# Kernel tuning notes

Measured on AMD Instinct MI355X. Metric: run time of the kernel, lower is better.

Reference implementation:

```python
import jax, jax.numpy as jnp
import numpy as np

K = 20
EPS = 1e-5


def _knn_idx(x, k):
    # x: (B, C, N) -> indices of k nearest neighbors (B, N, k)
    xx = jnp.sum(x * x, axis=1)                       # (B, N)
    inner = jnp.einsum('bcn,bcm->bnm', x, x)          # (B, N, N)
    pd = -xx[:, :, None] + 2.0 * inner - xx[:, None, :]  # negative sq dist
    return jax.lax.top_k(pd, k)[1]


def _graph_feature(x, k):
    # x: (B, C, N) -> (B, 2C, N, k) edge features [x_j - x_i, x_i]
    B = x.shape[0]
    idx = _knn_idx(x, k)                              # (B, N, k)
    xt = jnp.transpose(x, (0, 2, 1))                  # (B, N, C)
    feat = xt[jnp.arange(B)[:, None, None], idx]      # (B, N, k, C)
    center = jnp.broadcast_to(xt[:, :, None, :], feat.shape)
    e = jnp.concatenate([feat - center, center], axis=-1)
    return jnp.transpose(e, (0, 3, 1, 2))


def _bn2d(x, g, b):
    # training-mode BatchNorm2d: stats over (B, N, k)
    m = x.mean(axis=(0, 2, 3), keepdims=True)
    v = x.var(axis=(0, 2, 3), keepdims=True)
    return (x - m) / jnp.sqrt(v + EPS) * g[None, :, None, None] + b[None, :, None, None]


def _gn(x, g, b, groups):
    # GroupNorm on (B, C, N)
    B, C, N = x.shape
    xr = x.reshape(B, groups, C // groups, N)
    m = xr.mean(axis=(2, 3), keepdims=True)
    v = xr.var(axis=(2, 3), keepdims=True)
    xn = ((xr - m) / jnp.sqrt(v + EPS)).reshape(B, C, N)
    return xn * g[None, :, None] + b[None, :, None]


def _lrelu(x):
    return jnp.where(x >= 0, x, 0.2 * x)


def _edge_block(x, W, g, b, k):
    # kNN graph -> 1x1 conv -> BN -> LeakyReLU -> max over neighbors
    e = _graph_feature(x, k)                          # (B, 2C, N, k)
    y = jnp.einsum('oc,bcnk->bonk', W, e)
    return _lrelu(_bn2d(y, g, b)).max(axis=-1)        # (B, O, N)


def _encoder(x, W1, g1, b1, W2, g2, b2, W3, g3, b3, W4, g4, b4, W5, g5, b5,
             Wm1, bm1, gm1, hm1, Wm2, bm2, gm2, hm2, Wm3, bm3, gm3, hm3):
    B, _, N = x.shape
    x1 = _edge_block(x,  W1, g1, b1, K)               # (B,  64, N)
    x2 = _edge_block(x1, W2, g2, b2, K)               # (B,  64, N)
    x3 = _edge_block(x2, W3, g3, b3, K)               # (B, 128, N)
    x4 = _edge_block(x3, W4, g4, b4, K)               # (B, 256, N)
    loc = jnp.concatenate([x1, x2, x3, x4], axis=1)   # (B, 512, N)
    y = _lrelu(_gn(jnp.einsum('oc,bcn->bon', W5, loc), g5, b5, 32))  # (B,256,N)
    glb = jnp.concatenate([y.max(axis=-1), y.mean(axis=-1)], axis=1)  # (B,512)
    rep = jnp.broadcast_to(glb[:, :, None], (B, glb.shape[1], N))
    z = jnp.concatenate([loc, rep], axis=1)           # (B, 1024, N)
    z = jax.nn.relu(_gn(jnp.einsum('oc,bcn->bon', Wm1, z) + bm1[None, :, None], gm1, hm1, 32))
    z = jax.nn.relu(_gn(jnp.einsum('oc,bcn->bon', Wm2, z) + bm2[None, :, None], gm2, hm2, 32))
    emb = jax.nn.relu(_gn(jnp.einsum('oc,bcn->bon', Wm3, z) + bm3[None, :, None], gm3, hm3, 32))
    return emb, glb[:, :, None]


def setup_inputs():
    key = jax.random.key(0)
    ks = jax.random.split(key, 12)
    B, N = 8, 2048
    d = {}
    d['transpose_xyz'] = jax.random.normal(ks[0], (B, 3, N), dtype=jnp.float32)
    def w(k, o, c):
        return jax.random.normal(k, (o, c), dtype=jnp.float32) * (1.0 / np.sqrt(c).astype(np.float32))
    d['W1'] = w(ks[1], 64, 6);    d['g1'] = jnp.ones((64,), jnp.float32);  d['b1'] = jnp.zeros((64,), jnp.float32)
    d['W2'] = w(ks[2], 64, 128);  d['g2'] = jnp.ones((64,), jnp.float32);  d['b2'] = jnp.zeros((64,), jnp.float32)
    d['W3'] = w(ks[3], 128, 128); d['g3'] = jnp.ones((128,), jnp.float32); d['b3'] = jnp.zeros((128,), jnp.float32)
    d['W4'] = w(ks[4], 256, 256); d['g4'] = jnp.ones((256,), jnp.float32); d['b4'] = jnp.zeros((256,), jnp.float32)
    d['W5'] = w(ks[5], 256, 512); d['g5'] = jnp.ones((256,), jnp.float32); d['b5'] = jnp.zeros((256,), jnp.float32)
    d['Wm1'] = w(ks[6], 512, 1024); d['bm1'] = jnp.zeros((512,), jnp.float32); d['gm1'] = jnp.ones((512,), jnp.float32); d['hm1'] = jnp.zeros((512,), jnp.float32)
    d['Wm2'] = w(ks[7], 256, 512);  d['bm2'] = jnp.zeros((256,), jnp.float32); d['gm2'] = jnp.ones((256,), jnp.float32); d['hm2'] = jnp.zeros((256,), jnp.float32)
    d['Wm3'] = w(ks[8], 128, 256);  d['bm3'] = jnp.zeros((128,), jnp.float32); d['gm3'] = jnp.ones((128,), jnp.float32); d['hm3'] = jnp.zeros((128,), jnp.float32)
    return d


def reference(transpose_xyz, W1, g1, b1, W2, g2, b2, W3, g3, b3, W4, g4, b4,
              W5, g5, b5, Wm1, bm1, gm1, hm1, Wm2, bm2, gm2, hm2, Wm3, bm3, gm3, hm3):
    return _encoder(transpose_xyz, W1, g1, b1, W2, g2, b2, W3, g3, b3, W4, g4, b4,
                    W5, g5, b5, Wm1, bm1, gm1, hm1, Wm2, bm2, gm2, hm2, Wm3, bm3, gm3, hm3)
```

## Files before the change

kernel.cpp:

```cpp
#include <hip/hip_runtime.h>
#include <math.h>

#define B_SZ 8
#define NP   2048
#define KNN  20
#define CNT_F 327680.0f

#define OB_LOC   0ull
#define OB_RB    33554432ull
#define OB_RC    75497472ull
#define OB_RD    92274688ull
#define OB_X0    100663296ull
#define OB_XX    100925440ull
#define OB_STD   100990976ull
#define OB_STI   102301696ull
#define OB_PS    103612416ull
#define OB_MEAN  103613440ull
#define OB_VAR   103613568ull
#define OB_GLB   103613696ull
#define OB_T1    103630080ull
#define OB_GM    103646464ull
#define OB_GR    103647488ull

__global__ __launch_bounds__(256) void k_prep(const float* __restrict__ xin, float* __restrict__ x0) {
    int t = blockIdx.x * 256 + threadIdx.x;
    if (t >= B_SZ * NP) return;
    int b = t >> 11, n = t & 2047;
    const float* s = xin + (size_t)b * 3 * NP + n;
    ((float4*)x0)[t] = make_float4(s[0], s[NP], s[2 * NP], 0.f);
}

template <int C>
__global__ __launch_bounds__(256) void k_xx(const float* __restrict__ x, int rs, float* __restrict__ xx) {
    int t = blockIdx.x * 256 + threadIdx.x;
    if (t >= B_SZ * NP) return;
    const float* p = x + (size_t)t * rs;
    float s = 0.f;
    for (int c = 0; c < C; ++c) s = __fadd_rn(s, __fmul_rn(p[c], p[c]));
    xx[t] = s;
}

__global__ __launch_bounds__(256) void k_pds(const float* __restrict__ x, int rs, int K,
                                             const float* __restrict__ xx, int j0,
                                             float* __restrict__ S) {
    __shared__ float Xs[16][132];
    __shared__ float Ws[16][132];
    int b = blockIdx.z;
    int m0 = blockIdx.x * 128, o0 = blockIdx.y * 128;
    const float* xb = x + (size_t)b * NP * rs;
    const float* xcb = xb + (size_t)(j0 + o0) * rs;
    int tid = threadIdx.x;
    int tx = tid & 15, ty = tid >> 4;
    float acc[8][8] = {};
    for (int k0 = 0; k0 < K; k0 += 16) {
        __syncthreads();
#pragma unroll
        for (int i = 0; i < 8; ++i) {
            int e = tid + i * 256;
            int kk = e & 15, mm = e >> 4;
            int k = k0 + kk;
            Xs[kk][mm] = (k < K) ? xb[(size_t)(m0 + mm) * rs + k] : 0.f;
            Ws[kk][mm] = (k < K) ? xcb[(size_t)mm * rs + k] : 0.f;
        }
        __syncthreads();
#pragma unroll
        for (int kk = 0; kk < 16; ++kk) {
            float4 a0 = *(const float4*)&Xs[kk][ty * 8];
            float4 a1 = *(const float4*)&Xs[kk][ty * 8 + 4];
            float4 b0 = *(const float4*)&Ws[kk][tx * 8];
            float4 b1 = *(const float4*)&Ws[kk][tx * 8 + 4];
            float av[8] = {a0.x, a0.y, a0.z, a0.w, a1.x, a1.y, a1.z, a1.w};
            float bv[8] = {b0.x, b0.y, b0.z, b0.w, b1.x, b1.y, b1.z, b1.w};
#pragma unroll
            for (int i = 0; i < 8; ++i)
#pragma unroll
                for (int j = 0; j < 8; ++j)
                    acc[i][j] = __fadd_rn(acc[i][j], __fmul_rn(av[i], bv[j]));
        }
    }
    const float* xxb = xx + b * NP;
#pragma unroll
    for (int i = 0; i < 8; ++i) {
        int m = m0 + ty * 8 + i;
        float nxx = -xxb[m];
        float* Sr = S + ((size_t)(b * NP + m)) * 512;
#pragma unroll
        for (int j = 0; j < 8; ++j) {
            int o = o0 + tx * 8 + j;
            float t2 = __fadd_rn(nxx, __fmul_rn(2.0f, acc[i][j]));
            Sr[o] = __fsub_rn(t2, xxb[j0 + o]);
        }
    }
}

__device__ __forceinline__ void tk_insert(float (&kd)[KNN], int (&ki)[KNN], float d, int j) {
    if (d <= kd[KNN - 1]) return;
#pragma unroll
    for (int t = 0; t < KNN; ++t) {
        if (d > kd[t]) { float td = kd[t]; kd[t] = d; d = td; int tj = ki[t]; ki[t] = j; j = tj; }
    }
}

__global__ __launch_bounds__(256) void k_topk(const float* __restrict__ S, float* __restrict__ std_,
                                              int* __restrict__ sti, int j0) {
    int tid = threadIdx.x;
    int row = blockIdx.x * 16 + (tid >> 4);
    int sub = tid & 15;
    float kd[KNN]; int ki[KNN];
#pragma unroll
    for (int t = 0; t < KNN; ++t) { kd[t] = -INFINITY; ki[t] = 0x7fffffff; }
    if (j0 != 0) {
        for (int t = sub; t < KNN; t += 16)
            tk_insert(kd, ki, std_[(size_t)row * KNN + t], sti[(size_t)row * KNN + t]);
    }
    const float* Sr = S + (size_t)row * 512;
    for (int q0 = sub * 4; q0 < 512; q0 += 64) {
        float4 d4 = *(const float4*)&Sr[q0];
        tk_insert(kd, ki, d4.x, j0 + q0 + 0);
        tk_insert(kd, ki, d4.y, j0 + q0 + 1);
        tk_insert(kd, ki, d4.z, j0 + q0 + 2);
        tk_insert(kd, ki, d4.w, j0 + q0 + 3);
    }
    for (int it = 0; it < KNN; ++it) {
        float v = kd[0]; int vi = ki[0];
#pragma unroll
        for (int m = 1; m < 16; m <<= 1) {
            float ov = __shfl_xor(v, m, 16);
            int ovi = __shfl_xor(vi, m, 16);
            if (ov > v || (ov == v && ovi < vi)) { v = ov; vi = ovi; }
        }
        if (sub == 0) { std_[(size_t)row * KNN + it] = v; sti[(size_t)row * KNN + it] = vi; }
        if (kd[0] == v && ki[0] == vi) {
#pragma unroll
            for (int t = 0; t < KNN - 1; ++t) { kd[t] = kd[t + 1]; ki[t] = ki[t + 1]; }
            kd[KNN - 1] = -INFINITY; ki[KNN - 1] = 0x7fffffff;
        }
    }
}

template <int C>
__global__ __launch_bounds__(256) void k_ymk(const float* __restrict__ x, int rs,
                                             const float* __restrict__ Wsl,
                                             const int* __restrict__ sti,
                                             float* __restrict__ ybuf) {
    __shared__ float Ws[32][2 * C + 1];
    __shared__ float Xj[KNN][C + 1];
    __shared__ float Xn[C];
    __shared__ int   sidx[KNN];
    int n = blockIdx.x, b = blockIdx.y;
    int tid = threadIdx.x;
    if (tid < KNN) sidx[tid] = sti[((size_t)b * NP + n) * KNN + tid];
    for (int e = tid; e < 32 * 2 * C; e += 256) {
        int o = e / (2 * C), c = e % (2 * C);
        Ws[o][c] = Wsl[(size_t)o * 2 * C + c];
    }
    if (tid < C) Xn[tid] = x[((size_t)b * NP + n) * rs + tid];
    __syncthreads();
    for (int e = tid; e < KNN * C; e += 256) {
        int k = e / C, c = e % C;
        Xj[k][c] = x[((size_t)b * NP + sidx[k]) * rs + c];
    }
    __syncthreads();
    int o = tid & 31;
    int kb = tid >> 5;
    int k0 = kb, k1 = kb + 8, k2 = kb + 16;
    int k2r = (k2 < KNN) ? k2 : 0;
    float a0 = 0.f, a1 = 0.f, a2 = 0.f;
    for (int c = 0; c < C; ++c) {
        float xnc = Xn[c];
        float w = Ws[o][c];
        a0 = __fadd_rn(a0, __fmul_rn(w, __fsub_rn(Xj[k0][c], xnc)));
        a1 = __fadd_rn(a1, __fmul_rn(w, __fsub_rn(Xj[k1][c], xnc)));
        a2 = __fadd_rn(a2, __fmul_rn(w, __fsub_rn(Xj[k2r][c], xnc)));
    }
    for (int c = 0; c < C; ++c) {
        float xnc = Xn[c];
        float w = Ws[o][C + c];
        a0 = __fadd_rn(a0, __fmul_rn(w, xnc));
        a1 = __fadd_rn(a1, __fmul_rn(w, xnc));
        a2 = __fadd_rn(a2, __fmul_rn(w, xnc));
    }
    size_t base = ((size_t)(b * 32 + o) * NP + n) * KNN;
    ybuf[base + k0] = a0;
    ybuf[base + k1] = a1;
    if (k2 < KNN) ybuf[base + k2] = a2;
}

__global__ __launch_bounds__(256) void k_pwsum(const float* __restrict__ ybuf,
                                               const float* __restrict__ meanv, int vmode,
                                               float* __restrict__ psum) {
    __shared__ float ns[64];
    int tid = threadIdx.x;
    int task = blockIdx.x;
    int o = task & 31;
    float m = vmode ? meanv[o] : 0.f;
    int wave = tid >> 6, lane = tid & 63;
    int leafj = lane >> 3, slot = lane & 7;
    const float* tb = ybuf + (size_t)task * (NP * KNN);
    for (int itg = 0; itg < 16; ++itg) {
        int g = itg * 4 + wave;
        const float* a = tb + g * 640 + leafj * 80 + slot;
        float v0 = a[0];
        if (vmode) { float t = __fsub_rn(v0, m); v0 = __fmul_rn(t, t); }
        float r = v0;
#pragma unroll
        for (int i = 1; i < 10; ++i) {
            float v = a[i * 8];
            if (vmode) { float t = __fsub_rn(v, m); v = __fmul_rn(t, t); }
            r = __fadd_rn(r, v);
        }
#pragma unroll
        for (int msk = 1; msk < 64; msk <<= 1)
            r = __fadd_rn(r, __shfl_xor(r, msk));
        if (lane == 0) ns[g] = r;
    }
    __syncthreads();
    if (tid < 64) {
        float v = ns[tid];
#pragma unroll
        for (int msk = 1; msk < 64; msk <<= 1)
            v = __fadd_rn(v, __shfl_xor(v, msk));
        if (tid == 0) psum[task] = v;
    }
}

__global__ __launch_bounds__(64) void k_comb(const float* __restrict__ psum, float* __restrict__ outv) {
    int o = threadIdx.x;
    if (o >= 32) return;
    float tot = psum[o];
    for (int b = 1; b < B_SZ; ++b) tot = __fadd_rn(tot, psum[b * 32 + o]);
    outv[o] = __fdiv_rn(tot, CNT_F);
}

__global__ __launch_bounds__(256) void k_xwrite(const float* __restrict__ ybuf,
                                                const float* __restrict__ meanv, const float* __restrict__ varv,
                                                const float* __restrict__ g, const float* __restrict__ bb,
                                                int coff, float* __restrict__ loc) {
    int t = blockIdx.x * 256 + threadIdx.x;
    int n = t & 2047;
    int o = (t >> 11) & 31;
    int b = t >> 16;
    if (b >= B_SZ) return;
    const float* yr = ybuf + ((size_t)(b * 32 + o) * NP + n) * KNN;
    float gv = g[o];
    float sel = yr[0];
    if (gv >= 0.f) { for (int k = 1; k < KNN; ++k) sel = fmaxf(sel, yr[k]); }
    else           { for (int k = 1; k < KNN; ++k) sel = fminf(sel, yr[k]); }
    float s = __fsqrt_rn(__fadd_rn(varv[o], 1e-5f));
    float d = __fdiv_rn(__fsub_rn(sel, meanv[o]), s);
    float z = __fadd_rn(__fmul_rn(d, gv), bb[o]);
    z = (z >= 0.f) ? z : __fmul_rn(0.2f, z);
    loc[((size_t)b * NP + n) * 512 + coff + o] = z;
}

__global__ __launch_bounds__(256) void enc_gemm(
    const float* __restrict__ X, long long bsX, int rsX,
    const float* __restrict__ W, int rsW, int K, int O,
    float* __restrict__ out, long long bsO, int rsO,
    const float* __restrict__ aux, long long bsA, int mode) {
    __shared__ float Xs[16][132];
    __shared__ float Ws[16][132];
    int b = blockIdx.z;
    int m0 = blockIdx.x * 128, o0 = blockIdx.y * 128;
    const float* Xb = X + (size_t)b * bsX;
    int tid = threadIdx.x;
    int tx = tid & 15, ty = tid >> 4;
    float acc[8][8] = {};
    for (int k0 = 0; k0 < K; k0 += 16) {
        __syncthreads();
#pragma unroll
        for (int i = 0; i < 8; ++i) {
            int e = tid + i * 256;
            int kk = e & 15, mm = e >> 4;
            int k = k0 + kk;
            Xs[kk][mm] = (k < K) ? Xb[(size_t)(m0 + mm) * rsX + k] : 0.f;
        }
#pragma unroll
        for (int i = 0; i < 8; ++i) {
            int e = tid + i * 256;
            int kk = e & 15, oo = e >> 4;
            int k = k0 + kk, o = o0 + oo;
            Ws[kk][oo] = (k < K && o < O) ? W[(size_t)o * rsW + k] : 0.f;
        }
        __syncthreads();
#pragma unroll
        for (int kk = 0; kk < 16; ++kk) {
            float4 a0 = *(const float4*)&Xs[kk][ty * 8];
            float4 a1 = *(const float4*)&Xs[kk][ty * 8 + 4];
            float4 b0 = *(const float4*)&Ws[kk][tx * 8];
            float4 b1 = *(const float4*)&Ws[kk][tx * 8 + 4];
            float av[8] = {a0.x, a0.y, a0.z, a0.w, a1.x, a1.y, a1.z, a1.w};
            float bv[8] = {b0.x, b0.y, b0.z, b0.w, b1.x, b1.y, b1.z, b1.w};
#pragma unroll
            for (int i = 0; i < 8; ++i)
#pragma unroll
                for (int j = 0; j < 8; ++j)
                    acc[i][j] += av[i] * bv[j];
        }
    }
    float* ob = out + (size_t)b * bsO;
    const float* ax = aux ? aux + (size_t)b * bsA : nullptr;
#pragma unroll
    for (int i = 0; i < 8; ++i) {
        int m = m0 + ty * 8 + i;
#pragma unroll
        for (int j = 0; j < 8; ++j) {
            int o = o0 + tx * 8 + j;
            if (o < O) {
                float val = acc[i][j];
                if (mode == 1) val += ax[o];
                ob[(size_t)m * rsO + o] = val;
            }
        }
    }
}

__global__ __launch_bounds__(256) void enc_gn5(const float* __restrict__ y, const float* __restrict__ g5,
                                               const float* __restrict__ b5, float* __restrict__ glb) {
    int b = blockIdx.y, g = blockIdx.x;
    int tid = threadIdx.x;
    const float* yb = y + (size_t)b * NP * 256 + g * 8;
    float s1 = 0.f, s2 = 0.f;
    for (int e = tid; e < NP * 8; e += 256) {
        int n = e >> 3, c = e & 7;
        float x = yb[(size_t)n * 256 + c];
        s1 += x; s2 += x * x;
    }
    __shared__ float rbuf[16];
#pragma unroll
    for (int m = 32; m >= 1; m >>= 1) { s1 += __shfl_xor(s1, m, 64); s2 += __shfl_xor(s2, m, 64); }
    if ((tid & 63) == 0) { rbuf[tid >> 6] = s1; rbuf[8 + (tid >> 6)] = s2; }
    __syncthreads();
    float S1 = rbuf[0] + rbuf[1] + rbuf[2] + rbuf[3];
    float S2 = rbuf[8] + rbuf[9] + rbuf[10] + rbuf[11];
    float mean = S1 / (float)(NP * 8);
    float var = S2 / (float)(NP * 8) - mean * mean;
    float rstd = rsqrtf(var + 1e-5f);
    int c = tid & 7;
    float gam = g5[g * 8 + c], bet = b5[g * 8 + c];
    float mx = -INFINITY, sum = 0.f;
    for (int e = tid; e < NP * 8; e += 256) {
        int n = e >> 3;
        float x = yb[(size_t)n * 256 + c];
        float z = (x - mean) * rstd * gam + bet;
        z = (z >= 0.f) ? z : 0.2f * z;
        mx = fmaxf(mx, z); sum += z;
    }
    __shared__ float smx[256], ssm[256];
    smx[tid] = mx; ssm[tid] = sum;
    __syncthreads();
    if (tid < 8) {
        float M = -INFINITY, S = 0.f;
        for (int i = tid; i < 256; i += 8) { M = fmaxf(M, smx[i]); S += ssm[i]; }
        glb[b * 512 + g * 8 + tid] = M;
        glb[b * 512 + 256 + g * 8 + tid] = S / (float)NP;
    }
}

__global__ __launch_bounds__(128) void enc_t1(const float* __restrict__ Wm1, const float* __restrict__ bm1,
                                              const float* __restrict__ glb, float* __restrict__ t1) {
    int b = blockIdx.y;
    int o = blockIdx.x * 128 + threadIdx.x;
    __shared__ float sg[512];
    for (int i = threadIdx.x; i < 512; i += 128) sg[i] = glb[b * 512 + i];
    __syncthreads();
    const float* wr = Wm1 + (size_t)o * 1024 + 512;
    float s = bm1[o];
    for (int c = 0; c < 512; ++c) s += wr[c] * sg[c];
    t1[b * 512 + o] = s;
}

__global__ __launch_bounds__(256) void enc_gnstats(const float* __restrict__ y, int C, int cgshift,
                                                   float* __restrict__ gmean, float* __restrict__ grstd) {
    int b = blockIdx.y, g = blockIdx.x;
    int Cg = 1 << cgshift;
    int tid = threadIdx.x;
    const float* yb = y + (size_t)b * NP * C + g * Cg;
    int tot = NP << cgshift;
    float s1 = 0.f, s2 = 0.f;
    for (int e = tid; e < tot; e += 256) {
        int n = e >> cgshift, c = e & (Cg - 1);
        float x = yb[(size_t)n * C + c];
        s1 += x; s2 += x * x;
    }
    __shared__ float rbuf[16];
#pragma unroll
    for (int m = 32; m >= 1; m >>= 1) { s1 += __shfl_xor(s1, m, 64); s2 += __shfl_xor(s2, m, 64); }
    if ((tid & 63) == 0) { rbuf[tid >> 6] = s1; rbuf[8 + (tid >> 6)] = s2; }
    __syncthreads();
    if (tid == 0) {
        float S1 = rbuf[0] + rbuf[1] + rbuf[2] + rbuf[3];
        float S2 = rbuf[8] + rbuf[9] + rbuf[10] + rbuf[11];
        float mean = S1 / (float)tot;
        float var = S2 / (float)tot - mean * mean;
        gmean[b * 32 + g] = mean;
        grstd[b * 32 + g] = rsqrtf(var + 1e-5f);
    }
}

__global__ __launch_bounds__(256) void enc_gnapply(float* __restrict__ y, int C, int cgshift, int bshift,
                                                   const float* __restrict__ gam, const float* __restrict__ bet,
                                                   const float* __restrict__ gmean, const float* __restrict__ grstd) {
    int t = blockIdx.x * 256 + threadIdx.x;
    if (t >= B_SZ * NP * C) return;
    int c = t & (C - 1);
    int b = t >> bshift;
    int g = c >> cgshift;
    float m = gmean[b * 32 + g], r = grstd[b * 32 + g];
    float z = (y[t] - m) * r * gam[c] + bet[c];
    y[t] = (z >= 0.f) ? z : 0.f;
}

__global__ void enc_out(const float* __restrict__ emb, float* __restrict__ out) {
    __shared__ float tile[32][33];
    int b = blockIdx.z;
    int n0 = blockIdx.x * 32, c0 = blockIdx.y * 32;
    int tx = threadIdx.x, ty = threadIdx.y;
    for (int i = ty; i < 32; i += 8)
        tile[i][tx] = emb[((size_t)b * NP + n0 + i) * 128 + c0 + tx];
    __syncthreads();
    for (int i = ty; i < 32; i += 8)
        out[((size_t)b * 128 + c0 + i) * NP + n0 + tx] = tile[tx][i];
}

__global__ __launch_bounds__(256) void enc_outglb(const float* __restrict__ glb, float* __restrict__ out) {
    int t = blockIdx.x * 256 + threadIdx.x;
    if (t < B_SZ * 512) out[2097152 + t] = glb[t];
}

extern "C" void kernel_launch(void* const* d_in, const int* in_sizes, int n_in,
                              void* d_out, int out_size, void* d_ws, size_t ws_size,
                              hipStream_t stream) {
    (void)in_sizes; (void)n_in; (void)out_size; (void)ws_size;
    const float* xin = (const float*)d_in[0];
    const float* W1 = (const float*)d_in[1];  const float* g1 = (const float*)d_in[2];  const float* b1 = (const float*)d_in[3];
    const float* W2 = (const float*)d_in[4];  const float* g2 = (const float*)d_in[5];  const float* b2 = (const float*)d_in[6];
    const float* W3 = (const float*)d_in[7];  const float* g3 = (const float*)d_in[8];  const float* b3 = (const float*)d_in[9];
    const float* W4 = (const float*)d_in[10]; const float* g4 = (const float*)d_in[11]; const float* b4 = (const float*)d_in[12];
    const float* W5 = (const float*)d_in[13]; const float* g5 = (const float*)d_in[14]; const float* b5 = (const float*)d_in[15];
    const float* Wm1 = (const float*)d_in[16]; const float* bm1 = (const float*)d_in[17];
    const float* gm1 = (const float*)d_in[18]; const float* hm1 = (const float*)d_in[19];
    const float* Wm2 = (const float*)d_in[20]; const float* bm2 = (const float*)d_in[21];
    const float* gm2 = (const float*)d_in[22]; const float* hm2 = (const float*)d_in[23];
    const float* Wm3 = (const float*)d_in[24]; const float* bm3 = (const float*)d_in[25];
    const float* gm3 = (const float*)d_in[26]; const float* hm3 = (const float*)d_in[27];
    float* out = (float*)d_out;
    char* base = (char*)d_ws;

    float* loc   = (float*)(base + OB_LOC);
    float* S     = (float*)(base + OB_RB);
    float* ybuf  = (float*)(base + OB_RB);
    float* z1    = (float*)(base + OB_RB);
    float* y5    = (float*)(base + OB_RC);
    float* z2    = (float*)(base + OB_RC);
    float* emb   = (float*)(base + OB_RD);
    float* x0    = (float*)(base + OB_X0);
    float* xx    = (float*)(base + OB_XX);
    float* std_  = (float*)(base + OB_STD);
    int*   sti   = (int*)  (base + OB_STI);
    float* psum  = (float*)(base + OB_PS);
    float* meanv = (float*)(base + OB_MEAN);
    float* varv  = (float*)(base + OB_VAR);
    float* glb   = (float*)(base + OB_GLB);
    float* t1    = (float*)(base + OB_T1);
    float* gm    = (float*)(base + OB_GM);
    float* gr    = (float*)(base + OB_GR);

    k_prep<<<64, 256, 0, stream>>>(xin, x0);

    struct LY { const float* x; int rs; int C; const float* W; int O;
                const float* g; const float* bb; int coff; };
    LY L[4] = {
        {x0,        4,   3,   W1, 64,  g1, b1, 0},
        {loc,       512, 64,  W2, 64,  g2, b2, 64},
        {loc + 64,  512, 64,  W3, 128, g3, b3, 128},
        {loc + 128, 512, 128, W4, 256, g4, b4, 256},
    };

    for (int l = 0; l < 4; ++l) {
        const LY& e = L[l];
        if (e.C == 3)       k_xx<3><<<64, 256, 0, stream>>>(e.x, e.rs, xx);
        else if (e.C == 64) k_xx<64><<<64, 256, 0, stream>>>(e.x, e.rs, xx);
        else                k_xx<128><<<64, 256, 0, stream>>>(e.x, e.rs, xx);
        for (int s = 0; s < 4; ++s) {
            k_pds<<<dim3(16, 4, B_SZ), 256, 0, stream>>>(e.x, e.rs, e.C, xx, s * 512, S);
            k_topk<<<1024, 256, 0, stream>>>(S, std_, sti, s * 512);
        }
        for (int o0 = 0; o0 < e.O; o0 += 32) {
            const float* Wsl = e.W + (size_t)o0 * 2 * e.C;
            dim3 gym(NP, B_SZ);
            if (e.C == 3)       k_ymk<3><<<gym, 256, 0, stream>>>(e.x, e.rs, Wsl, sti, ybuf);
            else if (e.C == 64) k_ymk<64><<<gym, 256, 0, stream>>>(e.x, e.rs, Wsl, sti, ybuf);
            else                k_ymk<128><<<gym, 256, 0, stream>>>(e.x, e.rs, Wsl, sti, ybuf);
            k_pwsum<<<256, 256, 0, stream>>>(ybuf, nullptr, 0, psum);
            k_comb<<<1, 64, 0, stream>>>(psum, meanv);
            k_pwsum<<<256, 256, 0, stream>>>(ybuf, meanv, 1, psum);
            k_comb<<<1, 64, 0, stream>>>(psum, varv);
            k_xwrite<<<(B_SZ * NP * 32) / 256, 256, 0, stream>>>(
                ybuf, meanv, varv, e.g + o0, e.bb + o0, e.coff + o0, loc);
        }
    }

    auto gemm = [&](const float* X, int rsX, const float* Wp, int rsW, int K, int O,
                    float* o_, int rsO, const float* aux, long long bsA, int mode) {
        dim3 g(NP / 128, (O + 127) / 128, B_SZ);
        enc_gemm<<<g, 256, 0, stream>>>(X, (long long)NP * rsX, rsX, Wp, rsW, K, O,
                                        o_, (long long)NP * rsO, rsO, aux, bsA, mode);
    };

    gemm(loc, 512, W5, 512, 512, 256, y5, 256, nullptr, 0, 0);
    enc_gn5<<<dim3(32, B_SZ), 256, 0, stream>>>(y5, g5, b5, glb);
    enc_t1<<<dim3(4, B_SZ), 128, 0, stream>>>(Wm1, bm1, glb, t1);

    gemm(loc, 512, Wm1, 1024, 512, 512, z1, 512, t1, 512, 1);
    enc_gnstats<<<dim3(32, B_SZ), 256, 0, stream>>>(z1, 512, 4, gm, gr);
    enc_gnapply<<<(B_SZ * NP * 512) / 256, 256, 0, stream>>>(z1, 512, 4, 20, gm1, hm1, gm, gr);

    gemm(z1, 512, Wm2, 512, 512, 256, z2, 256, bm2, 0, 1);
    enc_gnstats<<<dim3(32, B_SZ), 256, 0, stream>>>(z2, 256, 3, gm, gr);
    enc_gnapply<<<(B_SZ * NP * 256) / 256, 256, 0, stream>>>(z2, 256, 3, 19, gm2, hm2, gm, gr);

    gemm(z2, 256, Wm3, 256, 256, 128, emb, 128, bm3, 0, 1);
    enc_gnstats<<<dim3(32, B_SZ), 256, 0, stream>>>(emb, 128, 2, gm, gr);
    enc_gnapply<<<(B_SZ * NP * 128) / 256, 256, 0, stream>>>(emb, 128, 2, 18, gm3, hm3, gm, gr);

    enc_out<<<dim3(64, 4, B_SZ), dim3(32, 8), 0, stream>>>(emb, out);
    enc_outglb<<<16, 256, 0, stream>>>(glb, out);
}
```

Baseline: 8.276 ms.

## Raise parallelism in distance GEMM, top-k, BN partial sums; hoist edge difference

The pairwise-distance GEMM is templated on channel count and uses 64-row tiles, doubling the block count and avoiding wasted padded-K work for the 3-channel layer. Top-k now uses 32 lanes per row instead of 16, so each lane scans fewer candidates. The BN sum kernel splits each channel-batch task into four blocks, with the combine kernel reducing the partials. The edge conv precomputes x_j - x_i once in shared memory instead of per output channel. In exchange, the 32-lane shuffle merge costs more per row, the summation order in the BN reduction changes, and the partial sums now reuse the top-k distance buffer.

```diff
diff --git a/kernel.cpp b/kernel.cpp
--- a/kernel.cpp
+++ b/kernel.cpp
@@ -40,39 +40,40 @@
     xx[t] = s;
 }
 
-__global__ __launch_bounds__(256) void k_pds(const float* __restrict__ x, int rs, int K,
+template <int KT>
+__global__ __launch_bounds__(256) void k_pds(const float* __restrict__ x, int rs,
                                              const float* __restrict__ xx, int j0,
                                              float* __restrict__ S) {
-    __shared__ float Xs[16][132];
-    __shared__ float Ws[16][132];
+    constexpr int KS = (KT < 16) ? KT : 16;
+    __shared__ float Xs[KS][68];
+    __shared__ float Ws[KS][132];
     int b = blockIdx.z;
-    int m0 = blockIdx.x * 128, o0 = blockIdx.y * 128;
+    int m0 = blockIdx.x * 64, o0 = blockIdx.y * 128;
     const float* xb = x + (size_t)b * NP * rs;
     const float* xcb = xb + (size_t)(j0 + o0) * rs;
     int tid = threadIdx.x;
     int tx = tid & 15, ty = tid >> 4;
-    float acc[8][8] = {};
-    for (int k0 = 0; k0 < K; k0 += 16) {
+    float acc[4][8] = {};
+    for (int k0 = 0; k0 < KT; k0 += KS) {
         __syncthreads();
-#pragma unroll
-        for (int i = 0; i < 8; ++i) {
-            int e = tid + i * 256;
-            int kk = e & 15, mm = e >> 4;
-            int k = k0 + kk;
-            Xs[kk][mm] = (k < K) ? xb[(size_t)(m0 + mm) * rs + k] : 0.f;
-            Ws[kk][mm] = (k < K) ? xcb[(size_t)mm * rs + k] : 0.f;
+        for (int e = tid; e < KS * 64; e += 256) {
+            int kk = e % KS, mm = e / KS;
+            Xs[kk][mm] = xb[(size_t)(m0 + mm) * rs + k0 + kk];
+        }
+        for (int e = tid; e < KS * 128; e += 256) {
+            int kk = e % KS, oo = e / KS;
+            Ws[kk][oo] = xcb[(size_t)oo * rs + k0 + kk];
         }
         __syncthreads();
 #pragma unroll
-        for (int kk = 0; kk < 16; ++kk) {
-            float4 a0 = *(const float4*)&Xs[kk][ty * 8];
-            float4 a1 = *(const float4*)&Xs[kk][ty * 8 + 4];
+        for (int kk = 0; kk < KS; ++kk) {
+            float4 a4 = *(const float4*)&Xs[kk][ty * 4];
             float4 b0 = *(const float4*)&Ws[kk][tx * 8];
             float4 b1 = *(const float4*)&Ws[kk][tx * 8 + 4];
-            float av[8] = {a0.x, a0.y, a0.z, a0.w, a1.x, a1.y, a1.z, a1.w};
+            float av[4] = {a4.x, a4.y, a4.z, a4.w};
             float bv[8] = {b0.x, b0.y, b0.z, b0.w, b1.x, b1.y, b1.z, b1.w};
 #pragma unroll
-            for (int i = 0; i < 8; ++i)
+            for (int i = 0; i < 4; ++i)
 #pragma unroll
                 for (int j = 0; j < 8; ++j)
                     acc[i][j] = __fadd_rn(acc[i][j], __fmul_rn(av[i], bv[j]));
@@ -80,8 +81,8 @@
     }
     const float* xxb = xx + b * NP;
 #pragma unroll
-    for (int i = 0; i < 8; ++i) {
-        int m = m0 + ty * 8 + i;
+    for (int i = 0; i < 4; ++i) {
+        int m = m0 + ty * 4 + i;
         float nxx = -xxb[m];
         float* Sr = S + ((size_t)(b * NP + m)) * 512;
 #pragma unroll
@@ -104,17 +105,17 @@
 __global__ __launch_bounds__(256) void k_topk(const float* __restrict__ S, float* __restrict__ std_,
                                               int* __restrict__ sti, int j0) {
     int tid = threadIdx.x;
-    int row = blockIdx.x * 16 + (tid >> 4);
-    int sub = tid & 15;
+    int row = blockIdx.x * 8 + (tid >> 5);
+    int sub = tid & 31;
     float kd[KNN]; int ki[KNN];
 #pragma unroll
     for (int t = 0; t < KNN; ++t) { kd[t] = -INFINITY; ki[t] = 0x7fffffff; }
     if (j0 != 0) {
-        for (int t = sub; t < KNN; t += 16)
+        for (int t = sub; t < KNN; t += 32)
             tk_insert(kd, ki, std_[(size_t)row * KNN + t], sti[(size_t)row * KNN + t]);
     }
     const float* Sr = S + (size_t)row * 512;
-    for (int q0 = sub * 4; q0 < 512; q0 += 64) {
+    for (int q0 = sub * 4; q0 < 512; q0 += 128) {
         float4 d4 = *(const float4*)&Sr[q0];
         tk_insert(kd, ki, d4.x, j0 + q0 + 0);
         tk_insert(kd, ki, d4.y, j0 + q0 + 1);
@@ -124,9 +125,9 @@
     for (int it = 0; it < KNN; ++it) {
         float v = kd[0]; int vi = ki[0];
 #pragma unroll
-        for (int m = 1; m < 16; m <<= 1) {
-            float ov = __shfl_xor(v, m, 16);
-            int ovi = __shfl_xor(vi, m, 16);
+        for (int m = 1; m < 32; m <<= 1) {
+            float ov = __shfl_xor(v, m, 32);
+            int ovi = __shfl_xor(vi, m, 32);
             if (ov > v || (ov == v && ovi < vi)) { v = ov; vi = ovi; }
         }
         if (sub == 0) { std_[(size_t)row * KNN + it] = v; sti[(size_t)row * KNN + it] = vi; }
@@ -144,7 +145,7 @@
                                              const int* __restrict__ sti,
                                              float* __restrict__ ybuf) {
     __shared__ float Ws[32][2 * C + 1];
-    __shared__ float Xj[KNN][C + 1];
+    __shared__ float Xd[KNN][C + 1];
     __shared__ float Xn[C];
     __shared__ int   sidx[KNN];
     int n = blockIdx.x, b = blockIdx.y;
@@ -158,7 +159,7 @@
     __syncthreads();
     for (int e = tid; e < KNN * C; e += 256) {
         int k = e / C, c = e % C;
-        Xj[k][c] = x[((size_t)b * NP + sidx[k]) * rs + c];
+        Xd[k][c] = __fsub_rn(x[((size_t)b * NP + sidx[k]) * rs + c], Xn[c]);
     }
     __syncthreads();
     int o = tid & 31;
@@ -167,18 +168,16 @@
     int k2r = (k2 < KNN) ? k2 : 0;
     float a0 = 0.f, a1 = 0.f, a2 = 0.f;
     for (int c = 0; c < C; ++c) {
-        float xnc = Xn[c];
         float w = Ws[o][c];
-        a0 = __fadd_rn(a0, __fmul_rn(w, __fsub_rn(Xj[k0][c], xnc)));
-        a1 = __fadd_rn(a1, __fmul_rn(w, __fsub_rn(Xj[k1][c], xnc)));
-        a2 = __fadd_rn(a2, __fmul_rn(w, __fsub_rn(Xj[k2r][c], xnc)));
+        a0 = __fadd_rn(a0, __fmul_rn(w, Xd[k0][c]));
+        a1 = __fadd_rn(a1, __fmul_rn(w, Xd[k1][c]));
+        a2 = __fadd_rn(a2, __fmul_rn(w, Xd[k2r][c]));
     }
     for (int c = 0; c < C; ++c) {
-        float xnc = Xn[c];
-        float w = Ws[o][C + c];
-        a0 = __fadd_rn(a0, __fmul_rn(w, xnc));
-        a1 = __fadd_rn(a1, __fmul_rn(w, xnc));
-        a2 = __fadd_rn(a2, __fmul_rn(w, xnc));
+        float p = __fmul_rn(Ws[o][C + c], Xn[c]);
+        a0 = __fadd_rn(a0, p);
+        a1 = __fadd_rn(a1, p);
+        a2 = __fadd_rn(a2, p);
     }
     size_t base = ((size_t)(b * 32 + o) * NP + n) * KNN;
     ybuf[base + k0] = a0;
@@ -188,16 +187,18 @@
 
 __global__ __launch_bounds__(256) void k_pwsum(const float* __restrict__ ybuf,
                                                const float* __restrict__ meanv, int vmode,
-                                               float* __restrict__ psum) {
-    __shared__ float ns[64];
-    int tid = threadIdx.x;
-    int task = blockIdx.x;
+                                               float* __restrict__ psum2) {
+    __shared__ float ns[16];
+    int tid = threadIdx.x;
+    int blk = blockIdx.x;
+    int task = blk >> 2;
+    int part = blk & 3;
     int o = task & 31;
     float m = vmode ? meanv[o] : 0.f;
     int wave = tid >> 6, lane = tid & 63;
     int leafj = lane >> 3, slot = lane & 7;
-    const float* tb = ybuf + (size_t)task * (NP * KNN);
-    for (int itg = 0; itg < 16; ++itg) {
+    const float* tb = ybuf + (size_t)task * (NP * KNN) + (size_t)part * 16 * 640;
+    for (int itg = 0; itg < 4; ++itg) {
         int g = itg * 4 + wave;
         const float* a = tb + g * 640 + leafj * 80 + slot;
         float v0 = a[0];
@@ -215,20 +216,24 @@
         if (lane == 0) ns[g] = r;
     }
     __syncthreads();
-    if (tid < 64) {
+    if (tid < 16) {
         float v = ns[tid];
 #pragma unroll
-        for (int msk = 1; msk < 64; msk <<= 1)
-            v = __fadd_rn(v, __shfl_xor(v, msk));
-        if (tid == 0) psum[task] = v;
-    }
-}
-
-__global__ __launch_bounds__(64) void k_comb(const float* __restrict__ psum, float* __restrict__ outv) {
+        for (int msk = 1; msk < 16; msk <<= 1)
+            v = __fadd_rn(v, __shfl_xor(v, msk, 16));
+        if (tid == 0) psum2[blk] = v;
+    }
+}
+
+__global__ __launch_bounds__(64) void k_comb(const float* __restrict__ psum2, float* __restrict__ outv) {
     int o = threadIdx.x;
     if (o >= 32) return;
-    float tot = psum[o];
-    for (int b = 1; b < B_SZ; ++b) tot = __fadd_rn(tot, psum[b * 32 + o]);
+    float tot = 0.f;
+    for (int b = 0; b < B_SZ; ++b) {
+        const float* p = psum2 + (size_t)(b * 32 + o) * 4;
+        float q = __fadd_rn(__fadd_rn(p[0], p[1]), __fadd_rn(p[2], p[3]));
+        tot = (b == 0) ? q : __fadd_rn(tot, q);
+    }
     outv[o] = __fdiv_rn(tot, CNT_F);
 }
 
@@ -457,8 +462,8 @@
     float* x0    = (float*)(base + OB_X0);
     float* xx    = (float*)(base + OB_XX);
     float* std_  = (float*)(base + OB_STD);
+    float* psum2 = (float*)(base + OB_STD);
     int*   sti   = (int*)  (base + OB_STI);
-    float* psum  = (float*)(base + OB_PS);
     float* meanv = (float*)(base + OB_MEAN);
     float* varv  = (float*)(base + OB_VAR);
     float* glb   = (float*)(base + OB_GLB);
@@ -482,9 +487,12 @@
         if (e.C == 3)       k_xx<3><<<64, 256, 0, stream>>>(e.x, e.rs, xx);
         else if (e.C == 64) k_xx<64><<<64, 256, 0, stream>>>(e.x, e.rs, xx);
         else                k_xx<128><<<64, 256, 0, stream>>>(e.x, e.rs, xx);
+        dim3 gp(32, 4, B_SZ);
         for (int s = 0; s < 4; ++s) {
-            k_pds<<<dim3(16, 4, B_SZ), 256, 0, stream>>>(e.x, e.rs, e.C, xx, s * 512, S);
-            k_topk<<<1024, 256, 0, stream>>>(S, std_, sti, s * 512);
+            if (e.C == 3)       k_pds<4><<<gp, 256, 0, stream>>>(e.x, e.rs, xx, s * 512, S);
+            else if (e.C == 64) k_pds<64><<<gp, 256, 0, stream>>>(e.x, e.rs, xx, s * 512, S);
+            else                k_pds<128><<<gp, 256, 0, stream>>>(e.x, e.rs, xx, s * 512, S);
+            k_topk<<<2048, 256, 0, stream>>>(S, std_, sti, s * 512);
         }
         for (int o0 = 0; o0 < e.O; o0 += 32) {
             const float* Wsl = e.W + (size_t)o0 * 2 * e.C;
@@ -492,10 +500,10 @@
             if (e.C == 3)       k_ymk<3><<<gym, 256, 0, stream>>>(e.x, e.rs, Wsl, sti, ybuf);
             else if (e.C == 64) k_ymk<64><<<gym, 256, 0, stream>>>(e.x, e.rs, Wsl, sti, ybuf);
             else                k_ymk<128><<<gym, 256, 0, stream>>>(e.x, e.rs, Wsl, sti, ybuf);
-            k_pwsum<<<256, 256, 0, stream>>>(ybuf, nullptr, 0, psum);
-            k_comb<<<1, 64, 0, stream>>>(psum, meanv);
-            k_pwsum<<<256, 256, 0, stream>>>(ybuf, meanv, 1, psum);
-            k_comb<<<1, 64, 0, stream>>>(psum, varv);
+            k_pwsum<<<1024, 256, 0, stream>>>(ybuf, nullptr, 0, psum2);
+            k_comb<<<1, 64, 0, stream>>>(psum2, meanv);
+            k_pwsum<<<1024, 256, 0, stream>>>(ybuf, meanv, 1, psum2);
+            k_comb<<<1, 64, 0, stream>>>(psum2, varv);
             k_xwrite<<<(B_SZ * NP * 32) / 256, 256, 0, stream>>>(
                 ybuf, meanv, varv, e.g + o0, e.bb + o0, e.coff + o0, loc);
         }
```

Result: faster. 7.759 ms (-6.2%).
